# Kernel optimization log

Hardware: AMD Instinct MI355X
Metric: run time of the kernel (lower is better)

Reference implementation:

```python
import jax, jax.numpy as jnp
import numpy as np

B, T, D, H, F = 2, 128, 256, 8, 64
C = H * F          # channels = 512
TEMB = 512         # time_embed_dim


def setup_inputs() -> dict:
    key = jax.random.key(0)
    ks = jax.random.split(key, 9)
    qk = jax.random.normal(ks[0], (B, D, H, T, F), jnp.float32)
    # integer-valued relative distances in [-(T-1), T-1], stored as float
    pairwise_distances = jax.random.randint(ks[1], (B, T, T), -(T - 1), T).astype(jnp.float32)
    temb = jax.random.normal(ks[2], (B, T, TEMB), jnp.float32)
    # linear layer params (note: original zero-inits w_out/b_out; we use random
    # values so the kernel correctness test is non-trivial)
    w_dist = jax.random.normal(ks[3], (C, 3), jnp.float32) / np.sqrt(3.0)
    b_dist = jax.random.normal(ks[4], (C,), jnp.float32) * 0.02
    w_time = jax.random.normal(ks[5], (C, TEMB), jnp.float32) / np.sqrt(TEMB)
    b_time = jax.random.normal(ks[6], (C,), jnp.float32) * 0.02
    w_out = jax.random.normal(ks[7], (C, C), jnp.float32) / np.sqrt(C)
    b_out = jax.random.normal(ks[8], (C,), jnp.float32) * 0.02
    return {"qk": qk, "pairwise_distances": pairwise_distances, "temb": temb,
            "w_dist": w_dist, "b_dist": b_dist, "w_time": w_time, "b_time": b_time,
            "w_out": w_out, "b_out": b_out}


def _rpe_net(pd, temb, w_dist, b_dist, w_time, b_time, w_out, b_out):
    # distance features: [B,T,T,3]
    dist_embs = jnp.stack([
        jnp.log1p(jnp.maximum(pd, 0.0)),
        jnp.log1p(jnp.maximum(-pd, 0.0)),
        (pd == 0).astype(pd.dtype),
    ], axis=-1)
    # [B,T,1,C] + [B,T,T,C]
    temb_emb = jnp.einsum('btk,ck->btc', temb, w_time) + b_time
    emb = temb_emb[:, :, None, :] + jnp.einsum('btsk,ck->btsc', dist_embs, w_dist) + b_dist
    r = jnp.einsum('btsc,oc->btso', jax.nn.silu(emb), w_out) + b_out
    return r.reshape(B, T, T, H, F)  # [B,T,S,H,F]


def reference(qk, pairwise_distances, temb, w_dist, b_dist, w_time, b_time, w_out, b_out):
    R = _rpe_net(pairwise_distances, temb, w_dist, b_dist, w_time, b_time, w_out, b_out)
    # mode == 'qk'
    return jnp.einsum('bdhtf,btshf->bdhts', qk, R)
```

## Files before the change

kernel.cpp:

```cpp
#include <hip/hip_runtime.h>
#include <hip/hip_bf16.h>
#include <math.h>

typedef __attribute__((ext_vector_type(8))) short short8;
typedef __attribute__((ext_vector_type(4))) float f32x4;

#define B_    2
#define T_    128
#define D_    256
#define H_    8
#define F_    64
#define C_    512
#define TEMB_ 512

static __device__ __forceinline__ unsigned short f2bf(float f) {
  __hip_bfloat16 h = __float2bfloat16(f);
  return reinterpret_cast<unsigned short&>(h);
}
static __device__ __forceinline__ unsigned int pk2(float a, float b) {
  return (unsigned int)f2bf(a) | ((unsigned int)f2bf(b) << 16);
}

__global__ __launch_bounds__(256) void k_prep(
    const float* __restrict__ w_out, const float* __restrict__ w_dist,
    short* __restrict__ wsw, float* __restrict__ wdT)
{
  int gid = blockIdx.x * 256 + threadIdx.x;
  for (int s = gid; s < 32768; s += 16384) {
    int oi = s >> 10, rem = s & 1023, kjg = rem >> 6, l = rem & 63;
    int o = oi * 16 + (l & 15), c = kjg * 32 + (l >> 4) * 8;
    const float* src = w_out + (size_t)o * C_ + c;
    float4 a = *reinterpret_cast<const float4*>(src);
    float4 b = *reinterpret_cast<const float4*>(src + 4);
    uint4 v; v.x = pk2(a.x, a.y); v.y = pk2(a.z, a.w);
    v.z = pk2(b.x, b.y); v.w = pk2(b.z, b.w);
    *reinterpret_cast<uint4*>(wsw + (size_t)s * 8) = v;
  }
  if (gid < C_) {
    wdT[0 * C_ + gid] = w_dist[gid * 3 + 0];
    wdT[1 * C_ + gid] = w_dist[gid * 3 + 1];
    wdT[2 * C_ + gid] = w_dist[gid * 3 + 2];
  }
}

__global__ __launch_bounds__(256) void k_base(
    const float* __restrict__ temb, const float* __restrict__ w_time,
    const float* __restrict__ b_time, const float* __restrict__ b_dist,
    float* __restrict__ base)
{
  __shared__ float tt[32][64];
  __shared__ float wt[64][65];
  const int bt0 = blockIdx.x * 32;
  const int c0  = blockIdx.y * 64;
  const int tid = threadIdx.x;
  const int cl  = tid & 63;
  const int g   = tid >> 6;
  float acc[8] = {0.f,0.f,0.f,0.f,0.f,0.f,0.f,0.f};

  for (int k0 = 0; k0 < TEMB_; k0 += 64) {
#pragma unroll
    for (int i = 0; i < 8; ++i) {
      int idx = tid + i * 256; int r = idx >> 6, k = idx & 63;
      tt[r][k] = temb[(size_t)(bt0 + r) * TEMB_ + k0 + k];
    }
#pragma unroll
    for (int i = 0; i < 16; ++i) {
      int idx = tid + i * 256; int r = idx >> 6, k = idx & 63;
      wt[r][k] = w_time[(size_t)(c0 + r) * TEMB_ + k0 + k];
    }
    __syncthreads();
#pragma unroll
    for (int k = 0; k < 64; ++k) {
      float w = wt[cl][k];
#pragma unroll
      for (int j = 0; j < 8; ++j) acc[j] += tt[g + 4 * j][k] * w;
    }
    __syncthreads();
  }
  float bb = b_time[c0 + cl] + b_dist[c0 + cl];
#pragma unroll
  for (int j = 0; j < 8; ++j)
    base[(size_t)(bt0 + g + 4 * j) * C_ + c0 + cl] = acc[j] + bb;
}

__global__ __launch_bounds__(1024, 4) void k_fused(
    const float* __restrict__ qk, const float* __restrict__ pd,
    const float* __restrict__ base, const float* __restrict__ wdT,
    const short* __restrict__ wsw, const float* __restrict__ b_out,
    float* __restrict__ out)
{
  __shared__ __align__(16) unsigned short Rlds[T_ * C_];
  __shared__ __align__(16) short At[8192];
  __shared__ float df[3][T_];

  const int bt = blockIdx.x;
  const int b  = bt >> 7;
  const int t  = bt & 127;
  const int tid  = threadIdx.x;
  const int lane = tid & 63;
  const int wave = tid >> 6;
  const int lanem = lane & 15;
  const int laneg = lane >> 4;

  if (tid < T_) {
    float p = pd[((size_t)b * T_ + t) * T_ + tid];
    df[0][tid] = log1pf(fmaxf(p, 0.f));
    df[1][tid] = log1pf(fmaxf(-p, 0.f));
    df[2][tid] = (p == 0.f) ? 1.f : 0.f;
  }

  const int wm = wave >> 3;
  const int wn = wave & 7;
  const int s_low = tid & 15;
  const int cg    = (tid >> 4) & 7;
  const int si    = tid >> 7;
  const int kjA   = cg >> 2;
  const int cgl   = cg & 3;
  const int laneslotA = s_low + 16 * cgl;
  const int sA    = si * 16 + s_low;
  const float* baserow = base + (size_t)bt * C_;

  f32x4 acc[4][4];
#pragma unroll
  for (int mi = 0; mi < 4; ++mi)
#pragma unroll
    for (int ni = 0; ni < 4; ++ni) acc[mi][ni] = (f32x4){0.f, 0.f, 0.f, 0.f};

  for (int kt = 0; kt < 8; ++kt) {
    __syncthreads();
    short8 b0[4], b1[4];
#pragma unroll
    for (int ni = 0; ni < 4; ++ni)
      b0[ni] = *reinterpret_cast<const short8*>(
          wsw + ((size_t)((wn * 4 + ni) * 16 + kt * 2 + 0) * 64 + lane) * 8);
    {
      const int cglob = kt * 64 + cg * 8;
      const float d0 = df[0][sA], d1 = df[1][sA], d2 = df[2][sA];
      uint4 v;
      {
        float4 bs = *reinterpret_cast<const float4*>(baserow + cglob);
        float4 wa = *reinterpret_cast<const float4*>(wdT + cglob);
        float4 wb = *reinterpret_cast<const float4*>(wdT + C_ + cglob);
        float4 wc = *reinterpret_cast<const float4*>(wdT + 2 * C_ + cglob);
        float x0 = bs.x + d0 * wa.x + d1 * wb.x + d2 * wc.x;
        float x1 = bs.y + d0 * wa.y + d1 * wb.y + d2 * wc.y;
        float x2 = bs.z + d0 * wa.z + d1 * wb.z + d2 * wc.z;
        float x3 = bs.w + d0 * wa.w + d1 * wb.w + d2 * wc.w;
        x0 = x0 / (1.f + __expf(-x0)); x1 = x1 / (1.f + __expf(-x1));
        x2 = x2 / (1.f + __expf(-x2)); x3 = x3 / (1.f + __expf(-x3));
        v.x = pk2(x0, x1); v.y = pk2(x2, x3);
      }
      {
        float4 bs = *reinterpret_cast<const float4*>(baserow + cglob + 4);
        float4 wa = *reinterpret_cast<const float4*>(wdT + cglob + 4);
        float4 wb = *reinterpret_cast<const float4*>(wdT + C_ + cglob + 4);
        float4 wc = *reinterpret_cast<const float4*>(wdT + 2 * C_ + cglob + 4);
        float x0 = bs.x + d0 * wa.x + d1 * wb.x + d2 * wc.x;
        float x1 = bs.y + d0 * wa.y + d1 * wb.y + d2 * wc.y;
        float x2 = bs.z + d0 * wa.z + d1 * wb.z + d2 * wc.z;
        float x3 = bs.w + d0 * wa.w + d1 * wb.w + d2 * wc.w;
        x0 = x0 / (1.f + __expf(-x0)); x1 = x1 / (1.f + __expf(-x1));
        x2 = x2 / (1.f + __expf(-x2)); x3 = x3 / (1.f + __expf(-x3));
        v.z = pk2(x0, x1); v.w = pk2(x2, x3);
      }
      *reinterpret_cast<uint4*>(&At[((si * 2 + kjA) * 64 + laneslotA) * 8]) = v;
    }
#pragma unroll
    for (int ni = 0; ni < 4; ++ni)
      b1[ni] = *reinterpret_cast<const short8*>(
          wsw + ((size_t)((wn * 4 + ni) * 16 + kt * 2 + 1) * 64 + lane) * 8);
    __syncthreads();
    {
      short8 a[4];
#pragma unroll
      for (int mi = 0; mi < 4; ++mi)
        a[mi] = *reinterpret_cast<const short8*>(
            &At[(((wm * 4 + mi) * 2 + 0) * 64 + lane) * 8]);
#pragma unroll
      for (int ni = 0; ni < 4; ++ni)
#pragma unroll
        for (int mi = 0; mi < 4; ++mi)
          acc[mi][ni] = __builtin_amdgcn_mfma_f32_16x16x32_bf16(
              a[mi], b0[ni], acc[mi][ni], 0, 0, 0);
#pragma unroll
      for (int mi = 0; mi < 4; ++mi)
        a[mi] = *reinterpret_cast<const short8*>(
            &At[(((wm * 4 + mi) * 2 + 1) * 64 + lane) * 8]);
#pragma unroll
      for (int ni = 0; ni < 4; ++ni)
#pragma unroll
        for (int mi = 0; mi < 4; ++mi)
          acc[mi][ni] = __builtin_amdgcn_mfma_f32_16x16x32_bf16(
              a[mi], b1[ni], acc[mi][ni], 0, 0, 0);
    }
  }

#pragma unroll
  for (int ni = 0; ni < 4; ++ni) {
    const int o  = wn * 64 + ni * 16 + lanem;
    const float bo = b_out[o];
    const int g  = o >> 3;
#pragma unroll
    for (int mi = 0; mi < 4; ++mi) {
#pragma unroll
      for (int reg = 0; reg < 4; ++reg) {
        int s  = wm * 64 + mi * 16 + laneg * 4 + reg;
        int gp = (g & ~7) | ((g ^ s) & 7);
        Rlds[s * 512 + gp * 8 + (o & 7)] = f2bf(acc[mi][ni][reg] + bo);
      }
    }
  }

  const int h  = wave >> 1;
  const int dh = wave & 1;
  const size_t HTF = (size_t)H_ * T_ * F_;
  const size_t HTT = (size_t)H_ * T_ * T_;
  const float* qkb = qk + (size_t)b * D_ * HTF + (size_t)h * T_ * F_ + (size_t)t * F_;
  float* outb = out + (size_t)b * D_ * HTT + (size_t)h * T_ * T_ + (size_t)t * T_;

  float4 buf[4];
  {
    const float* src = qkb + (size_t)(dh * 128 + lanem) * HTF + laneg * 8;
    buf[0] = *reinterpret_cast<const float4*>(src);
    buf[1] = *reinterpret_cast<const float4*>(src + 4);
    buf[2] = *reinterpret_cast<const float4*>(src + 32);
    buf[3] = *reinterpret_cast<const float4*>(src + 36);
  }
  __syncthreads();

  short8 brf[2][8];
#pragma unroll
  for (int kj = 0; kj < 2; ++kj)
#pragma unroll
    for (int ni = 0; ni < 8; ++ni) {
      int s  = ni * 16 + lanem;
      int g  = h * 8 + kj * 4 + laneg;
      int gp = (g & ~7) | ((g ^ s) & 7);
      brf[kj][ni] = *reinterpret_cast<const short8*>(&Rlds[s * 512 + gp * 8]);
    }
  __syncthreads();

  char* stO = (char*)Rlds + (size_t)wave * 8192;
  const int xw = lanem << 4;
  const int l5 = lane >> 5;
  const int sb = (lane & 31) * 16;

  for (int cc = 0; cc < 8; ++cc) {
    const int dbase = dh * 128 + cc * 16;
    short8 qb0, qb1;
    {
      union { uint4 u; short8 s; } cv;
      cv.u.x = pk2(buf[0].x, buf[0].y); cv.u.y = pk2(buf[0].z, buf[0].w);
      cv.u.z = pk2(buf[1].x, buf[1].y); cv.u.w = pk2(buf[1].z, buf[1].w);
      qb0 = cv.s;
      cv.u.x = pk2(buf[2].x, buf[2].y); cv.u.y = pk2(buf[2].z, buf[2].w);
      cv.u.z = pk2(buf[3].x, buf[3].y); cv.u.w = pk2(buf[3].z, buf[3].w);
      qb1 = cv.s;
    }
    if (cc < 7) {
      const float* src = qkb + (size_t)(dbase + 16 + lanem) * HTF + laneg * 8;
      buf[0] = *reinterpret_cast<const float4*>(src);
      buf[1] = *reinterpret_cast<const float4*>(src + 4);
      buf[2] = *reinterpret_cast<const float4*>(src + 32);
      buf[3] = *reinterpret_cast<const float4*>(src + 36);
    }
    f32x4 ac[8];
#pragma unroll
    for (int ni = 0; ni < 8; ++ni) ac[ni] = (f32x4){0.f, 0.f, 0.f, 0.f};
#pragma unroll
    for (int ni = 0; ni < 8; ++ni)
      ac[ni] = __builtin_amdgcn_mfma_f32_16x16x32_bf16(brf[0][ni], qb0, ac[ni], 0, 0, 0);
#pragma unroll
    for (int ni = 0; ni < 8; ++ni)
      ac[ni] = __builtin_amdgcn_mfma_f32_16x16x32_bf16(brf[1][ni], qb1, ac[ni], 0, 0, 0);
#pragma unroll
    for (int ni = 0; ni < 8; ++ni)
      *reinterpret_cast<f32x4*>(
          stO + lanem * 512 + ((ni * 64 + laneg * 16) ^ xw)) = ac[ni];
#pragma unroll
    for (int i = 0; i < 8; ++i) {
      int r = i * 2 + l5;
      float4 v = *reinterpret_cast<const float4*>(
          stO + r * 512 + (sb ^ (r << 4)));
      *reinterpret_cast<float4*>(
          outb + (size_t)(dbase + r) * HTT + (lane & 31) * 4) = v;
    }
  }
}

extern "C" void kernel_launch(void* const* d_in, const int* in_sizes, int n_in,
                              void* d_out, int out_size, void* d_ws, size_t ws_size,
                              hipStream_t stream) {
  const float* qk     = (const float*)d_in[0];
  const float* pd     = (const float*)d_in[1];
  const float* temb   = (const float*)d_in[2];
  const float* w_dist = (const float*)d_in[3];
  const float* b_dist = (const float*)d_in[4];
  const float* w_time = (const float*)d_in[5];
  const float* b_time = (const float*)d_in[6];
  const float* w_out  = (const float*)d_in[7];
  const float* b_out  = (const float*)d_in[8];
  float* out = (float*)d_out;

  char* ws = (char*)d_ws;
  float* base = (float*)(ws);
  float* wdT  = (float*)(ws + 524288);
  short* wsw  = (short*)(ws + 532480);

  hipLaunchKernelGGL(k_prep, dim3(64), dim3(256), 0, stream,
                     w_out, w_dist, wsw, wdT);
  hipLaunchKernelGGL(k_base, dim3(8, 8), dim3(256), 0, stream,
                     temb, w_time, b_time, b_dist, base);
  hipLaunchKernelGGL(k_fused, dim3(B_ * T_), dim3(1024), 0, stream,
                     qk, pd, base, wdT, wsw, b_out, out);
}
```

Baseline: 192.1 us.

## Split fused kernel into RPE GEMM and QK contraction kernels via global R buffer

Merges the prep and base kernels into one launch. Splits the large 1024-thread fused kernel, whose 128 KB of R in LDS allowed only one block per CU, into two kernels. k_rpe computes half the output channels per block and writes bf16 R to a global workspace. k_qkr runs one block per (b,t,h) with small LDS staging, giving many more and smaller blocks. The aim is better occupancy and parallelism, at the cost of a global round-trip for R (about 33 MB of bf16) and one extra launch.

```diff
diff --git a/kernel.cpp b/kernel.cpp
--- a/kernel.cpp
+++ b/kernel.cpp
@@ -21,38 +21,36 @@
   return (unsigned int)f2bf(a) | ((unsigned int)f2bf(b) << 16);
 }
 
-__global__ __launch_bounds__(256) void k_prep(
-    const float* __restrict__ w_out, const float* __restrict__ w_dist,
-    short* __restrict__ wsw, float* __restrict__ wdT)
-{
-  int gid = blockIdx.x * 256 + threadIdx.x;
-  for (int s = gid; s < 32768; s += 16384) {
-    int oi = s >> 10, rem = s & 1023, kjg = rem >> 6, l = rem & 63;
-    int o = oi * 16 + (l & 15), c = kjg * 32 + (l >> 4) * 8;
-    const float* src = w_out + (size_t)o * C_ + c;
-    float4 a = *reinterpret_cast<const float4*>(src);
-    float4 b = *reinterpret_cast<const float4*>(src + 4);
-    uint4 v; v.x = pk2(a.x, a.y); v.y = pk2(a.z, a.w);
-    v.z = pk2(b.x, b.y); v.w = pk2(b.z, b.w);
-    *reinterpret_cast<uint4*>(wsw + (size_t)s * 8) = v;
-  }
-  if (gid < C_) {
-    wdT[0 * C_ + gid] = w_dist[gid * 3 + 0];
-    wdT[1 * C_ + gid] = w_dist[gid * 3 + 1];
-    wdT[2 * C_ + gid] = w_dist[gid * 3 + 2];
-  }
-}
-
-__global__ __launch_bounds__(256) void k_base(
+__global__ __launch_bounds__(256) void k_pre(
     const float* __restrict__ temb, const float* __restrict__ w_time,
     const float* __restrict__ b_time, const float* __restrict__ b_dist,
-    float* __restrict__ base)
+    const float* __restrict__ w_out, const float* __restrict__ w_dist,
+    float* __restrict__ base, short* __restrict__ wsw, float* __restrict__ wdT)
 {
+  const int tid = threadIdx.x;
+  if (blockIdx.x >= 64) {
+    int gid = (blockIdx.x - 64) * 256 + tid;
+    for (int s = gid; s < 32768; s += 16384) {
+      int oi = s >> 10, rem = s & 1023, kjg = rem >> 6, l = rem & 63;
+      int o = oi * 16 + (l & 15), c = kjg * 32 + (l >> 4) * 8;
+      const float* src = w_out + (size_t)o * C_ + c;
+      float4 a = *reinterpret_cast<const float4*>(src);
+      float4 b = *reinterpret_cast<const float4*>(src + 4);
+      uint4 v; v.x = pk2(a.x, a.y); v.y = pk2(a.z, a.w);
+      v.z = pk2(b.x, b.y); v.w = pk2(b.z, b.w);
+      *reinterpret_cast<uint4*>(wsw + (size_t)s * 8) = v;
+    }
+    if (gid < C_) {
+      wdT[0 * C_ + gid] = w_dist[gid * 3 + 0];
+      wdT[1 * C_ + gid] = w_dist[gid * 3 + 1];
+      wdT[2 * C_ + gid] = w_dist[gid * 3 + 2];
+    }
+    return;
+  }
   __shared__ float tt[32][64];
   __shared__ float wt[64][65];
-  const int bt0 = blockIdx.x * 32;
-  const int c0  = blockIdx.y * 64;
-  const int tid = threadIdx.x;
+  const int bt0 = (blockIdx.x & 7) * 32;
+  const int c0  = (blockIdx.x >> 3) * 64;
   const int cl  = tid & 63;
   const int g   = tid >> 6;
   float acc[8] = {0.f,0.f,0.f,0.f,0.f,0.f,0.f,0.f};
@@ -83,17 +81,151 @@
     base[(size_t)(bt0 + g + 4 * j) * C_ + c0 + cl] = acc[j] + bb;
 }
 
-__global__ __launch_bounds__(1024, 4) void k_fused(
-    const float* __restrict__ qk, const float* __restrict__ pd,
-    const float* __restrict__ base, const float* __restrict__ wdT,
-    const short* __restrict__ wsw, const float* __restrict__ b_out,
+__global__ __launch_bounds__(512, 4) void k_rpe(
+    const float* __restrict__ pd, const float* __restrict__ base,
+    const float* __restrict__ wdT, const short* __restrict__ wsw,
+    const float* __restrict__ b_out, unsigned short* __restrict__ Rg)
+{
+  __shared__ __align__(16) short At[8192];
+  __shared__ float df[3][T_];
+
+  const int bx   = blockIdx.x;
+  const int bt   = bx >> 1;
+  const int half = bx & 1;
+  const int b    = bt >> 7;
+  const int t    = bt & 127;
+  const int tid  = threadIdx.x;
+  const int lane = tid & 63;
+  const int wave = tid >> 6;
+  const int lanem = lane & 15;
+  const int laneg = lane >> 4;
+
+  if (tid < T_) {
+    float p = pd[((size_t)b * T_ + t) * T_ + tid];
+    df[0][tid] = log1pf(fmaxf(p, 0.f));
+    df[1][tid] = log1pf(fmaxf(-p, 0.f));
+    df[2][tid] = (p == 0.f) ? 1.f : 0.f;
+  }
+
+  const int wm = wave >> 2;
+  const int wn = wave & 3;
+  const int s_low = tid & 15;
+  const int cg    = (tid >> 4) & 7;
+  const int si_b  = (tid >> 7) * 2;
+  const int kjA   = cg >> 2;
+  const int cgl   = cg & 3;
+  const int laneslotA = s_low + 16 * cgl;
+  const float* baserow = base + (size_t)bt * C_;
+
+  f32x4 acc[4][4];
+#pragma unroll
+  for (int mi = 0; mi < 4; ++mi)
+#pragma unroll
+    for (int ni = 0; ni < 4; ++ni) acc[mi][ni] = (f32x4){0.f, 0.f, 0.f, 0.f};
+
+  for (int kt = 0; kt < 8; ++kt) {
+    __syncthreads();
+    short8 b0[4], b1[4];
+#pragma unroll
+    for (int ni = 0; ni < 4; ++ni) {
+      int oi = half * 16 + wn * 4 + ni;
+      b0[ni] = *reinterpret_cast<const short8*>(
+          wsw + ((size_t)(oi * 16 + kt * 2 + 0) * 64 + lane) * 8);
+    }
+    {
+      const int cglob = kt * 64 + cg * 8;
+      float4 bs0 = *reinterpret_cast<const float4*>(baserow + cglob);
+      float4 bs1 = *reinterpret_cast<const float4*>(baserow + cglob + 4);
+      float4 wa0 = *reinterpret_cast<const float4*>(wdT + cglob);
+      float4 wa1 = *reinterpret_cast<const float4*>(wdT + cglob + 4);
+      float4 wb0 = *reinterpret_cast<const float4*>(wdT + C_ + cglob);
+      float4 wb1 = *reinterpret_cast<const float4*>(wdT + C_ + cglob + 4);
+      float4 wc0 = *reinterpret_cast<const float4*>(wdT + 2 * C_ + cglob);
+      float4 wc1 = *reinterpret_cast<const float4*>(wdT + 2 * C_ + cglob + 4);
+#pragma unroll
+      for (int q = 0; q < 2; ++q) {
+        int si = si_b + q;
+        int s  = si * 16 + s_low;
+        float d0 = df[0][s], d1 = df[1][s], d2 = df[2][s];
+        uint4 v;
+        {
+          float x0 = bs0.x + d0 * wa0.x + d1 * wb0.x + d2 * wc0.x;
+          float x1 = bs0.y + d0 * wa0.y + d1 * wb0.y + d2 * wc0.y;
+          float x2 = bs0.z + d0 * wa0.z + d1 * wb0.z + d2 * wc0.z;
+          float x3 = bs0.w + d0 * wa0.w + d1 * wb0.w + d2 * wc0.w;
+          x0 = x0 / (1.f + __expf(-x0)); x1 = x1 / (1.f + __expf(-x1));
+          x2 = x2 / (1.f + __expf(-x2)); x3 = x3 / (1.f + __expf(-x3));
+          v.x = pk2(x0, x1); v.y = pk2(x2, x3);
+        }
+        {
+          float x0 = bs1.x + d0 * wa1.x + d1 * wb1.x + d2 * wc1.x;
+          float x1 = bs1.y + d0 * wa1.y + d1 * wb1.y + d2 * wc1.y;
+          float x2 = bs1.z + d0 * wa1.z + d1 * wb1.z + d2 * wc1.z;
+          float x3 = bs1.w + d0 * wa1.w + d1 * wb1.w + d2 * wc1.w;
+          x0 = x0 / (1.f + __expf(-x0)); x1 = x1 / (1.f + __expf(-x1));
+          x2 = x2 / (1.f + __expf(-x2)); x3 = x3 / (1.f + __expf(-x3));
+          v.z = pk2(x0, x1); v.w = pk2(x2, x3);
+        }
+        *reinterpret_cast<uint4*>(&At[((si * 2 + kjA) * 64 + laneslotA) * 8]) = v;
+      }
+    }
+#pragma unroll
+    for (int ni = 0; ni < 4; ++ni) {
+      int oi = half * 16 + wn * 4 + ni;
+      b1[ni] = *reinterpret_cast<const short8*>(
+          wsw + ((size_t)(oi * 16 + kt * 2 + 1) * 64 + lane) * 8);
+    }
+    __syncthreads();
+    {
+      short8 a[4];
+#pragma unroll
+      for (int mi = 0; mi < 4; ++mi)
+        a[mi] = *reinterpret_cast<const short8*>(
+            &At[(((wm * 4 + mi) * 2 + 0) * 64 + lane) * 8]);
+#pragma unroll
+      for (int ni = 0; ni < 4; ++ni)
+#pragma unroll
+        for (int mi = 0; mi < 4; ++mi)
+          acc[mi][ni] = __builtin_amdgcn_mfma_f32_16x16x32_bf16(
+              b0[ni], a[mi], acc[mi][ni], 0, 0, 0);
+#pragma unroll
+      for (int mi = 0; mi < 4; ++mi)
+        a[mi] = *reinterpret_cast<const short8*>(
+            &At[(((wm * 4 + mi) * 2 + 1) * 64 + lane) * 8]);
+#pragma unroll
+      for (int ni = 0; ni < 4; ++ni)
+#pragma unroll
+        for (int mi = 0; mi < 4; ++mi)
+          acc[mi][ni] = __builtin_amdgcn_mfma_f32_16x16x32_bf16(
+              b1[ni], a[mi], acc[mi][ni], 0, 0, 0);
+    }
+  }
+
+  unsigned short* Rbt = Rg + (size_t)bt * T_ * C_;
+#pragma unroll
+  for (int ni = 0; ni < 4; ++ni) {
+    const int o0 = half * 256 + wn * 64 + ni * 16 + laneg * 4;
+    const float4 bo4 = *reinterpret_cast<const float4*>(b_out + o0);
+#pragma unroll
+    for (int mi = 0; mi < 4; ++mi) {
+      const int s = wm * 64 + mi * 16 + lanem;
+      uint2 v;
+      v.x = pk2(acc[mi][ni][0] + bo4.x, acc[mi][ni][1] + bo4.y);
+      v.y = pk2(acc[mi][ni][2] + bo4.z, acc[mi][ni][3] + bo4.w);
+      *reinterpret_cast<uint2*>(Rbt + (size_t)s * C_ + o0) = v;
+    }
+  }
+}
+
+__global__ __launch_bounds__(256, 4) void k_qkr(
+    const float* __restrict__ qk, const unsigned short* __restrict__ Rg,
     float* __restrict__ out)
 {
-  __shared__ __align__(16) unsigned short Rlds[T_ * C_];
-  __shared__ __align__(16) short At[8192];
-  __shared__ float df[3][T_];
-
-  const int bt = blockIdx.x;
+  __shared__ __align__(16) float stage[4][2048];
+
+  const int bx = blockIdx.x;
+  const int h  = bx & 7;
+  const int bt = bx >> 3;
   const int b  = bt >> 7;
   const int t  = bt & 127;
   const int tid  = threadIdx.x;
@@ -101,152 +233,38 @@
   const int wave = tid >> 6;
   const int lanem = lane & 15;
   const int laneg = lane >> 4;
-
-  if (tid < T_) {
-    float p = pd[((size_t)b * T_ + t) * T_ + tid];
-    df[0][tid] = log1pf(fmaxf(p, 0.f));
-    df[1][tid] = log1pf(fmaxf(-p, 0.f));
-    df[2][tid] = (p == 0.f) ? 1.f : 0.f;
-  }
-
-  const int wm = wave >> 3;
-  const int wn = wave & 7;
-  const int s_low = tid & 15;
-  const int cg    = (tid >> 4) & 7;
-  const int si    = tid >> 7;
-  const int kjA   = cg >> 2;
-  const int cgl   = cg & 3;
-  const int laneslotA = s_low + 16 * cgl;
-  const int sA    = si * 16 + s_low;
-  const float* baserow = base + (size_t)bt * C_;
-
-  f32x4 acc[4][4];
-#pragma unroll
-  for (int mi = 0; mi < 4; ++mi)
-#pragma unroll
-    for (int ni = 0; ni < 4; ++ni) acc[mi][ni] = (f32x4){0.f, 0.f, 0.f, 0.f};
-
-  for (int kt = 0; kt < 8; ++kt) {
-    __syncthreads();
-    short8 b0[4], b1[4];
-#pragma unroll
-    for (int ni = 0; ni < 4; ++ni)
-      b0[ni] = *reinterpret_cast<const short8*>(
-          wsw + ((size_t)((wn * 4 + ni) * 16 + kt * 2 + 0) * 64 + lane) * 8);
-    {
-      const int cglob = kt * 64 + cg * 8;
-      const float d0 = df[0][sA], d1 = df[1][sA], d2 = df[2][sA];
-      uint4 v;
-      {
-        float4 bs = *reinterpret_cast<const float4*>(baserow + cglob);
-        float4 wa = *reinterpret_cast<const float4*>(wdT + cglob);
-        float4 wb = *reinterpret_cast<const float4*>(wdT + C_ + cglob);
-        float4 wc = *reinterpret_cast<const float4*>(wdT + 2 * C_ + cglob);
-        float x0 = bs.x + d0 * wa.x + d1 * wb.x + d2 * wc.x;
-        float x1 = bs.y + d0 * wa.y + d1 * wb.y + d2 * wc.y;
-        float x2 = bs.z + d0 * wa.z + d1 * wb.z + d2 * wc.z;
-        float x3 = bs.w + d0 * wa.w + d1 * wb.w + d2 * wc.w;
-        x0 = x0 / (1.f + __expf(-x0)); x1 = x1 / (1.f + __expf(-x1));
-        x2 = x2 / (1.f + __expf(-x2)); x3 = x3 / (1.f + __expf(-x3));
-        v.x = pk2(x0, x1); v.y = pk2(x2, x3);
-      }
-      {
-        float4 bs = *reinterpret_cast<const float4*>(baserow + cglob + 4);
-        float4 wa = *reinterpret_cast<const float4*>(wdT + cglob + 4);
-        float4 wb = *reinterpret_cast<const float4*>(wdT + C_ + cglob + 4);
-        float4 wc = *reinterpret_cast<const float4*>(wdT + 2 * C_ + cglob + 4);
-        float x0 = bs.x + d0 * wa.x + d1 * wb.x + d2 * wc.x;
-        float x1 = bs.y + d0 * wa.y + d1 * wb.y + d2 * wc.y;
-        float x2 = bs.z + d0 * wa.z + d1 * wb.z + d2 * wc.z;
-        float x3 = bs.w + d0 * wa.w + d1 * wb.w + d2 * wc.w;
-        x0 = x0 / (1.f + __expf(-x0)); x1 = x1 / (1.f + __expf(-x1));
-        x2 = x2 / (1.f + __expf(-x2)); x3 = x3 / (1.f + __expf(-x3));
-        v.z = pk2(x0, x1); v.w = pk2(x2, x3);
-      }
-      *reinterpret_cast<uint4*>(&At[((si * 2 + kjA) * 64 + laneslotA) * 8]) = v;
-    }
-#pragma unroll
-    for (int ni = 0; ni < 4; ++ni)
-      b1[ni] = *reinterpret_cast<const short8*>(
-          wsw + ((size_t)((wn * 4 + ni) * 16 + kt * 2 + 1) * 64 + lane) * 8);
-    __syncthreads();
-    {
-      short8 a[4];
-#pragma unroll
-      for (int mi = 0; mi < 4; ++mi)
-        a[mi] = *reinterpret_cast<const short8*>(
-            &At[(((wm * 4 + mi) * 2 + 0) * 64 + lane) * 8]);
-#pragma unroll
-      for (int ni = 0; ni < 4; ++ni)
-#pragma unroll
-        for (int mi = 0; mi < 4; ++mi)
-          acc[mi][ni] = __builtin_amdgcn_mfma_f32_16x16x32_bf16(
-              a[mi], b0[ni], acc[mi][ni], 0, 0, 0);
-#pragma unroll
-      for (int mi = 0; mi < 4; ++mi)
-        a[mi] = *reinterpret_cast<const short8*>(
-            &At[(((wm * 4 + mi) * 2 + 1) * 64 + lane) * 8]);
-#pragma unroll
-      for (int ni = 0; ni < 4; ++ni)
-#pragma unroll
-        for (int mi = 0; mi < 4; ++mi)
-          acc[mi][ni] = __builtin_amdgcn_mfma_f32_16x16x32_bf16(
-              a[mi], b1[ni], acc[mi][ni], 0, 0, 0);
-    }
-  }
-
-#pragma unroll
-  for (int ni = 0; ni < 4; ++ni) {
-    const int o  = wn * 64 + ni * 16 + lanem;
-    const float bo = b_out[o];
-    const int g  = o >> 3;
-#pragma unroll
-    for (int mi = 0; mi < 4; ++mi) {
-#pragma unroll
-      for (int reg = 0; reg < 4; ++reg) {
-        int s  = wm * 64 + mi * 16 + laneg * 4 + reg;
-        int gp = (g & ~7) | ((g ^ s) & 7);
-        Rlds[s * 512 + gp * 8 + (o & 7)] = f2bf(acc[mi][ni][reg] + bo);
-      }
-    }
-  }
-
-  const int h  = wave >> 1;
-  const int dh = wave & 1;
+  const int d0w = wave * 64;
+
   const size_t HTF = (size_t)H_ * T_ * F_;
   const size_t HTT = (size_t)H_ * T_ * T_;
   const float* qkb = qk + (size_t)b * D_ * HTF + (size_t)h * T_ * F_ + (size_t)t * F_;
   float* outb = out + (size_t)b * D_ * HTT + (size_t)h * T_ * T_ + (size_t)t * T_;
+  const unsigned short* Rb = Rg + (size_t)bt * T_ * C_ + h * F_;
 
   float4 buf[4];
   {
-    const float* src = qkb + (size_t)(dh * 128 + lanem) * HTF + laneg * 8;
+    const float* src = qkb + (size_t)(d0w + lanem) * HTF + laneg * 8;
     buf[0] = *reinterpret_cast<const float4*>(src);
     buf[1] = *reinterpret_cast<const float4*>(src + 4);
     buf[2] = *reinterpret_cast<const float4*>(src + 32);
     buf[3] = *reinterpret_cast<const float4*>(src + 36);
   }
-  __syncthreads();
 
   short8 brf[2][8];
 #pragma unroll
   for (int kj = 0; kj < 2; ++kj)
 #pragma unroll
-    for (int ni = 0; ni < 8; ++ni) {
-      int s  = ni * 16 + lanem;
-      int g  = h * 8 + kj * 4 + laneg;
-      int gp = (g & ~7) | ((g ^ s) & 7);
-      brf[kj][ni] = *reinterpret_cast<const short8*>(&Rlds[s * 512 + gp * 8]);
-    }
-  __syncthreads();
-
-  char* stO = (char*)Rlds + (size_t)wave * 8192;
+    for (int ni = 0; ni < 8; ++ni)
+      brf[kj][ni] = *reinterpret_cast<const short8*>(
+          Rb + (size_t)(ni * 16 + lanem) * C_ + kj * 32 + laneg * 8);
+
+  char* stO = (char*)stage[wave];
   const int xw = lanem << 4;
   const int l5 = lane >> 5;
   const int sb = (lane & 31) * 16;
 
-  for (int cc = 0; cc < 8; ++cc) {
-    const int dbase = dh * 128 + cc * 16;
+  for (int cc = 0; cc < 4; ++cc) {
+    const int dbase = d0w + cc * 16;
     short8 qb0, qb1;
     {
       union { uint4 u; short8 s; } cv;
@@ -257,7 +275,7 @@
       cv.u.z = pk2(buf[3].x, buf[3].y); cv.u.w = pk2(buf[3].z, buf[3].w);
       qb1 = cv.s;
     }
-    if (cc < 7) {
+    if (cc < 3) {
       const float* src = qkb + (size_t)(dbase + 16 + lanem) * HTF + laneg * 8;
       buf[0] = *reinterpret_cast<const float4*>(src);
       buf[1] = *reinterpret_cast<const float4*>(src + 4);
@@ -303,14 +321,16 @@
   float* out = (float*)d_out;
 
   char* ws = (char*)d_ws;
-  float* base = (float*)(ws);
-  float* wdT  = (float*)(ws + 524288);
-  short* wsw  = (short*)(ws + 532480);
-
-  hipLaunchKernelGGL(k_prep, dim3(64), dim3(256), 0, stream,
-                     w_out, w_dist, wsw, wdT);
-  hipLaunchKernelGGL(k_base, dim3(8, 8), dim3(256), 0, stream,
-                     temb, w_time, b_time, b_dist, base);
-  hipLaunchKernelGGL(k_fused, dim3(B_ * T_), dim3(1024), 0, stream,
-                     qk, pd, base, wdT, wsw, b_out, out);
-}
+  float* base          = (float*)(ws);
+  float* wdT           = (float*)(ws + 524288);
+  short* wsw           = (short*)(ws + 532480);
+  unsigned short* Rg   = (unsigned short*)(ws + 1056768);
+
+  hipLaunchKernelGGL(k_pre, dim3(128), dim3(256), 0, stream,
+                     temb, w_time, b_time, b_dist, w_out, w_dist,
+                     base, wsw, wdT);
+  hipLaunchKernelGGL(k_rpe, dim3(2 * B_ * T_), dim3(512), 0, stream,
+                     pd, base, wdT, wsw, b_out, Rg);
+  hipLaunchKernelGGL(k_qkr, dim3(B_ * T_ * H_), dim3(256), 0, stream,
+                     qk, Rg, out);
+}
```

After: 203.1 us. 1.06x slower.
